# Kernel tuning notes

Hardware: AMD Instinct MI355X
Metric: run time of the kernel (lower is better)

Reference implementation:

```python
import math
import jax, jax.numpy as jnp
import numpy as np

B, T, C = 2, 2048, 1024
N_HEAD = 16
HEAD_DIM = C // N_HEAD


def setup_inputs() -> dict:
    key = jax.random.key(0)
    k1, k2, k3 = jax.random.split(key, 3)
    x = jax.random.normal(k1, (B, T, C), dtype=jnp.float32)
    w_attn = jax.random.normal(k2, (3 * C, C), dtype=jnp.float32) * 0.02
    w_proj = jax.random.normal(k3, (C, C), dtype=jnp.float32) * 0.02
    return {"x": x, "w_attn": w_attn, "w_proj": w_proj}


def _rope_cos_sin(seq_len, dim, dtype):
    inv_freq = 1.0 / (10000.0 ** (jnp.arange(0, dim, 2, dtype=jnp.float32) / dim))
    t = jnp.arange(seq_len, dtype=jnp.float32)
    freqs = jnp.einsum('i,j->ij', t, inv_freq)          # [T, dim/2]
    emb = jnp.concatenate([freqs, freqs], axis=-1)       # [T, dim]
    return jnp.cos(emb).astype(dtype), jnp.sin(emb).astype(dtype)


def _rotate_half(x):
    x1, x2 = jnp.split(x, 2, axis=-1)
    return jnp.concatenate([-x2, x1], axis=-1)


def _apply_rope(x, cos, sin):
    # x: [B, H, T, D]; cos/sin: [T, D] broadcast over batch/head
    return x * cos[None, None] + _rotate_half(x) * sin[None, None]


def reference(x, w_attn, w_proj):
    b, t, c = x.shape
    h, d = N_HEAD, c // N_HEAD
    qkv = x @ w_attn.T                                   # [B, T, 3C]
    q, k, v = jnp.split(qkv, 3, axis=-1)
    q = q.reshape(b, t, h, d).transpose(0, 2, 1, 3)      # [B, H, T, D]
    k = k.reshape(b, t, h, d).transpose(0, 2, 1, 3)
    v = v.reshape(b, t, h, d).transpose(0, 2, 1, 3)
    cos, sin = _rope_cos_sin(t, d, x.dtype)
    q = _apply_rope(q, cos, sin)
    k = _apply_rope(k, cos, sin)
    logits = jnp.einsum('bhqd,bhkd->bhqk', q, k) * (1.0 / math.sqrt(d))
    causal = jnp.tril(jnp.ones((t, t), dtype=bool))
    logits = jnp.where(causal[None, None], logits, jnp.float32(-jnp.inf).astype(logits.dtype))
    att = jax.nn.softmax(logits, axis=-1)                # [B, H, T, T]
    y = jnp.einsum('bhqk,bhkd->bhqd', att, v)            # [B, H, T, D]
    y = y.transpose(0, 2, 1, 3).reshape(b, t, c)
    return y @ w_proj.T
```

## Files before the change

kernel.cpp:

```cpp
#include <hip/hip_runtime.h>
#include <hip/hip_bf16.h>
#include <math.h>

#define B_ 2
#define T_ 2048
#define C_ 1024
#define H_ 16

typedef __bf16 bf16x8 __attribute__((ext_vector_type(8)));
typedef __bf16 bf16x4 __attribute__((ext_vector_type(4)));
typedef float f32x4 __attribute__((ext_vector_type(4)));
typedef float f32x16 __attribute__((ext_vector_type(16)));
typedef unsigned int u32;

#if __has_builtin(__builtin_amdgcn_exp2f)
#define EXP2(x) __builtin_amdgcn_exp2f(x)
#else
#define EXP2(x) exp2f(x)
#endif

__device__ __forceinline__ void gload16(const void* g, void* l) {
    __builtin_amdgcn_global_load_lds(
        (const __attribute__((address_space(1))) void*)g,
        (__attribute__((address_space(3))) void*)l, 16, 0, 0);
}

__device__ __forceinline__ f32x4 mfma16(bf16x8 a, bf16x8 b, f32x4 c) {
    return __builtin_amdgcn_mfma_f32_16x16x32_bf16(a, b, c, 0, 0, 0);
}
__device__ __forceinline__ f32x16 mfma32(bf16x8 a, bf16x8 b, f32x16 c) {
    return __builtin_amdgcn_mfma_f32_32x32x16_bf16(a, b, c, 0, 0, 0);
}

__device__ __forceinline__ u32 cvtpk(float lo, float hi) {
    u32 r;
    asm("v_cvt_pk_bf16_f32 %0, %1, %2" : "=v"(r) : "v"(lo), "v"(hi));
    return r;
}

__device__ __forceinline__ void plane32swap(u32& a, u32& b) {
#if __has_builtin(__builtin_amdgcn_permlane32_swap)
    auto r = __builtin_amdgcn_permlane32_swap(a, b, false, false);
    a = r[0]; b = r[1];
#else
    asm("v_permlane32_swap_b32 %0, %1" : "+v"(a), "+v"(b));
#endif
}

#define SCLQ 0.18033688011112042f
#define NLOG2_10K_32 (-0.4152410118609203f)

__global__ __launch_bounds__(256) void cast_all(const float* __restrict__ x,
                                                const float* __restrict__ wa,
                                                const float* __restrict__ wp,
                                                __bf16* __restrict__ xb,
                                                __bf16* __restrict__ wab,
                                                __bf16* __restrict__ wpb) {
    const int i = blockIdx.x * 256 + threadIdx.x;
    const float* src;
    __bf16* dst;
    int k;
    if (i < 1048576)               { src = x;  dst = xb;  k = i; }
    else if (i < 1048576 + 786432) { src = wa; dst = wab; k = i - 1048576; }
    else                           { src = wp; dst = wpb; k = i - (1048576 + 786432); }
    float4 v = ((const float4*)src)[k];
    bf16x4 o;
    o[0] = (__bf16)v.x; o[1] = (__bf16)v.y; o[2] = (__bf16)v.z; o[3] = (__bf16)v.w;
    ((bf16x4*)dst)[k] = o;
}

__global__ __launch_bounds__(256) void gemm_qkv(const __bf16* __restrict__ A,
                                                const __bf16* __restrict__ Bw,
                                                __bf16* __restrict__ Qb,
                                                __bf16* __restrict__ Kb,
                                                __bf16* __restrict__ Vt) {
    const int tid  = threadIdx.x;
    const int lane = tid & 63;
    const int w    = tid >> 6;
    const int wr = w >> 1, wc = w & 1;
    const int l15 = lane & 15, lg = lane >> 4;
    const int bm = blockIdx.y * 128, bn = blockIdx.x * 128;
    const int K = C_;
    __shared__ __bf16 Asm[128 * 64];
    __shared__ __bf16 Bsm[128 * 64];
    f32x4 acc[4][4] = {};

    for (int kt = 0; kt < K; kt += 64) {
        if (kt) __syncthreads();
#pragma unroll
        for (int it = 0; it < 4; ++it) {
            const int c = it * 256 + tid;
            const int row = c >> 3, cc = (c & 7) * 8;
            gload16(A  + (size_t)(bm + row) * K + kt + cc, Asm + c * 8);
            gload16(Bw + (size_t)(bn + row) * K + kt + cc, Bsm + c * 8);
        }
        __syncthreads();
#pragma unroll
        for (int kk = 0; kk < 64; kk += 32) {
            bf16x8 af[4], bf[4];
#pragma unroll
            for (int i = 0; i < 4; ++i)
                af[i] = *(const bf16x8*)&Asm[(wr * 64 + i * 16 + l15) * 64 + kk + lg * 8];
#pragma unroll
            for (int j = 0; j < 4; ++j)
                bf[j] = *(const bf16x8*)&Bsm[(wc * 64 + j * 16 + l15) * 64 + kk + lg * 8];
#pragma unroll
            for (int i = 0; i < 4; ++i)
#pragma unroll
                for (int j = 0; j < 4; ++j)
                    acc[i][j] = mfma16(af[i], bf[j], acc[i][j]);
        }
    }
    const int region  = bn >> 10;
    const int colbase = (bn & 1023) + wc * 64;
    const int h = colbase >> 6;
    if (region < 2) {
        __bf16* dst = region ? Kb : Qb;
        const float scl = region ? 1.0f : SCLQ;
#pragma unroll
        for (int j = 0; j < 2; ++j) {
            const int d = j * 16 + l15;
            const float invf = exp2f((float)d * NLOG2_10K_32);
#pragma unroll
            for (int i = 0; i < 4; ++i)
#pragma unroll
                for (int r = 0; r < 4; ++r) {
                    const int row = bm + wr * 64 + i * 16 + lg * 4 + r;
                    const int b = row >> 11, t = row & (T_ - 1);
                    float sv, cv;
                    __sincosf((float)t * invf, &sv, &cv);
                    const float v1 = acc[i][j][r], v2 = acc[i][j + 2][r];
                    const float o1 = (v1 * cv - v2 * sv) * scl;
                    const float o2 = (v2 * cv + v1 * sv) * scl;
                    const size_t base = ((size_t)(b * H_ + h) * T_ + t) * 64;
                    dst[base + d]      = (__bf16)o1;
                    dst[base + d + 32] = (__bf16)o2;
                }
        }
    } else {
#pragma unroll
        for (int i = 0; i < 4; ++i)
#pragma unroll
            for (int j = 0; j < 4; ++j) {
                const int vcol = colbase + j * 16 + l15;
                const int hh = vcol >> 6, d = vcol & 63;
                const int row0 = bm + wr * 64 + i * 16 + lg * 4;
                const int b = row0 >> 11, t0 = row0 & (T_ - 1);
                u32 dw[2];
                dw[0] = cvtpk(acc[i][j][0], acc[i][j][1]);
                dw[1] = cvtpk(acc[i][j][2], acc[i][j][3]);
                *(uint64_t*)&Vt[((size_t)(b * H_ + hh) * 64 + d) * T_ + t0] =
                    *(uint64_t*)dw;
            }
    }
}

__global__ __launch_bounds__(256) void gemm_proj(const __bf16* __restrict__ A,
                                                 const __bf16* __restrict__ Bw,
                                                 float* __restrict__ Cp,
                                                 int N, int K) {
    const int tid  = threadIdx.x;
    const int lane = tid & 63;
    const int w    = tid >> 6;
    const int wr = w >> 1, wc = w & 1;
    const int l15 = lane & 15, lg = lane >> 4;
    const int bm = blockIdx.y * 128, bn = blockIdx.x * 128;
    __shared__ __bf16 Asm[128 * 64];
    __shared__ __bf16 Bsm[128 * 64];
    f32x4 acc[4][4] = {};

    for (int kt = 0; kt < K; kt += 64) {
        if (kt) __syncthreads();
#pragma unroll
        for (int it = 0; it < 4; ++it) {
            const int c = it * 256 + tid;
            const int row = c >> 3, cc = (c & 7) * 8;
            gload16(A  + (size_t)(bm + row) * K + kt + cc, Asm + c * 8);
            gload16(Bw + (size_t)(bn + row) * K + kt + cc, Bsm + c * 8);
        }
        __syncthreads();
#pragma unroll
        for (int kk = 0; kk < 64; kk += 32) {
            bf16x8 af[4], bf[4];
#pragma unroll
            for (int i = 0; i < 4; ++i)
                af[i] = *(const bf16x8*)&Asm[(wr * 64 + i * 16 + l15) * 64 + kk + lg * 8];
#pragma unroll
            for (int j = 0; j < 4; ++j)
                bf[j] = *(const bf16x8*)&Bsm[(wc * 64 + j * 16 + l15) * 64 + kk + lg * 8];
#pragma unroll
            for (int i = 0; i < 4; ++i)
#pragma unroll
                for (int j = 0; j < 4; ++j)
                    acc[i][j] = mfma16(af[i], bf[j], acc[i][j]);
        }
    }
#pragma unroll
    for (int i = 0; i < 4; ++i)
#pragma unroll
        for (int j = 0; j < 4; ++j)
#pragma unroll
            for (int r = 0; r < 4; ++r) {
                const int row = bm + wr * 64 + i * 16 + lg * 4 + r;
                const int col = bn + wc * 64 + j * 16 + l15;
                Cp[(size_t)row * N + col] = acc[i][j][r];
            }
}

__global__ __launch_bounds__(256) void attn_fwd(const __bf16* __restrict__ Qb,
                                                const __bf16* __restrict__ Kb,
                                                const __bf16* __restrict__ Vt,
                                                __bf16* __restrict__ Yatt) {
    const int gid = blockIdx.x;
    const int bh = (gid & 7) * 4 + ((gid >> 3) & 3);
    const int qt = 15 - (gid >> 5);
    const int b = bh >> 4, h = bh & 15;
    const int tid = threadIdx.x, lane = tid & 63, w = tid >> 6;
    const int l31 = lane & 31, hi = lane >> 5;
    const int hi4 = hi * 4;
    __shared__ __bf16 Ksm[128 * 64];
    __shared__ __bf16 Vsm[64 * 128];

    const int Q0 = qt * 128 + w * 32;
    const int qg = Q0 + l31;
    const __bf16* Qp = Qb + ((size_t)bh * T_ + Q0) * 64;
    const __bf16* Kp = Kb + (size_t)bh * T_ * 64;
    const __bf16* Vp = Vt + (size_t)bh * 64 * T_;

    bf16x8 qf[4];
#pragma unroll
    for (int ds = 0; ds < 4; ++ds)
        qf[ds] = *(const bf16x8*)&Qp[l31 * 64 + ds * 16 + hi * 8];

    f32x16 ot[2] = {};
    float m_run = -1e30f, l_run = 0.f;

    const int jmax = qt + 1;
    for (int j = 0; j < jmax; ++j) {
        __syncthreads();
#pragma unroll
        for (int it = 0; it < 4; ++it) {
            const int g = it * 256 + tid;
            const int kr = g >> 3, kc = (g & 7) ^ (kr & 7);
            gload16(Kp + ((size_t)(j * 128 + kr)) * 64 + kc * 8, Ksm + g * 8);
            const int vd = g >> 4, vg = (g & 15) ^ (vd & 15);
            gload16(Vp + (size_t)vd * T_ + j * 128 + vg * 8, Vsm + g * 8);
        }
        __syncthreads();

        f32x16 st[4] = {};
#pragma unroll
        for (int a = 0; a < 4; ++a)
#pragma unroll
            for (int ds = 0; ds < 4; ++ds) {
                const int row = a * 32 + l31;
                const int off = (ds * 32 + hi * 16) ^ ((row & 7) << 4);
                bf16x8 kf = *(const bf16x8*)((const char*)Ksm + row * 128 + off);
                st[a] = mfma32(kf, qf[ds], st[a]);
            }
        if (j == qt) {
#pragma unroll
            for (int a = 0; a < 4; ++a)
#pragma unroll
                for (int r = 0; r < 16; ++r) {
                    const int kv = j * 128 + a * 32 + (r & 3) + 8 * (r >> 2) + hi4;
                    if (kv > qg) st[a][r] = -1e30f;
                }
        }
        float t8[8];
#pragma unroll
        for (int i = 0; i < 8; ++i)
            t8[i] = fmaxf(fmaxf(fmaxf(st[0][i], st[0][i + 8]),
                                fmaxf(st[1][i], st[1][i + 8])),
                          fmaxf(fmaxf(st[2][i], st[2][i + 8]),
                                fmaxf(st[3][i], st[3][i + 8])));
        float mx = fmaxf(fmaxf(fmaxf(t8[0], t8[1]), fmaxf(t8[2], t8[3])),
                         fmaxf(fmaxf(t8[4], t8[5]), fmaxf(t8[6], t8[7])));
        mx = fmaxf(mx, __shfl_xor(mx, 32));
        if (!__all(mx - m_run <= 10.f)) {
            const float mnew = fmaxf(m_run, mx);
            const float corr = EXP2(m_run - mnew);
            l_run *= corr;
#pragma unroll
            for (int db = 0; db < 2; ++db)
#pragma unroll
                for (int r = 0; r < 16; ++r) ot[db][r] *= corr;
            m_run = mnew;
        }
        float s0 = 0.f, s1 = 0.f;
#pragma unroll
        for (int a = 0; a < 4; ++a)
#pragma unroll
            for (int r = 0; r < 16; ++r) {
                const float e = EXP2(st[a][r] - m_run);
                st[a][r] = e;
                if (r & 1) s1 += e; else s0 += e;
            }
        float rs = s0 + s1;
        rs += __shfl_xor(rs, 32);
        l_run += rs;
        bf16x8 pa[8];
#pragma unroll
        for (int ks = 0; ks < 8; ++ks) {
            const int a = ks >> 1, rb = (ks & 1) * 8;
            u32 X0 = cvtpk(st[a][rb + 0], st[a][rb + 1]);
            u32 X1 = cvtpk(st[a][rb + 2], st[a][rb + 3]);
            u32 Y0 = cvtpk(st[a][rb + 4], st[a][rb + 5]);
            u32 Y1 = cvtpk(st[a][rb + 6], st[a][rb + 7]);
            plane32swap(X0, Y0);
            plane32swap(X1, Y1);
            u32 dw[4] = {X0, X1, Y0, Y1};
            pa[ks] = *(bf16x8*)dw;
        }
#pragma unroll
        for (int ks = 0; ks < 8; ++ks)
#pragma unroll
            for (int db = 0; db < 2; ++db) {
                const int row = db * 32 + l31;
                const int off = ((ks * 2 + hi) ^ (row & 15)) * 16;
                bf16x8 vf = *(const bf16x8*)((const char*)Vsm + row * 256 + off);
                ot[db] = mfma32(vf, pa[ks], ot[db]);
            }
    }
    const float inv = 1.f / l_run;
    __bf16* Yp = Yatt + ((size_t)(b * T_ + qg)) * C_ + h * 64;
#pragma unroll
    for (int db = 0; db < 2; ++db)
#pragma unroll
        for (int rq = 0; rq < 4; ++rq) {
            const int r = rq * 4;
            u32 dw[2];
            dw[0] = cvtpk(ot[db][r] * inv,     ot[db][r + 1] * inv);
            dw[1] = cvtpk(ot[db][r + 2] * inv, ot[db][r + 3] * inv);
            const int d = db * 32 + 8 * rq + hi4;
            *(uint64_t*)&Yp[d] = *(uint64_t*)dw;
        }
}

extern "C" void kernel_launch(void* const* d_in, const int* in_sizes, int n_in,
                              void* d_out, int out_size, void* d_ws, size_t ws_size,
                              hipStream_t stream) {
    const float* x      = (const float*)d_in[0];
    const float* w_attn = (const float*)d_in[1];
    const float* w_proj = (const float*)d_in[2];
    float* out = (float*)d_out;
    char* ws = (char*)d_ws;

    __bf16* xb  = (__bf16*)(ws);
    __bf16* wab = (__bf16*)(ws + 8388608);
    __bf16* wpb = (__bf16*)(ws + 14680064);
    __bf16* Qb  = (__bf16*)(ws + 16777216);
    __bf16* Kb  = (__bf16*)(ws + 25165824);
    __bf16* Vt  = (__bf16*)(ws + 33554432);
    __bf16* Ya  = (__bf16*)(ws + 41943040);

    cast_all<<<dim3(8192), 256, 0, stream>>>(x, w_attn, w_proj, xb, wab, wpb);

    gemm_qkv<<<dim3(3 * C_ / 128, B_ * T_ / 128), 256, 0, stream>>>(
        xb, wab, Qb, Kb, Vt);

    attn_fwd<<<dim3(16 * 32), 256, 0, stream>>>(Qb, Kb, Vt, Ya);

    gemm_proj<<<dim3(C_ / 128, B_ * T_ / 128), 256, 0, stream>>>(
        Ya, wpb, out, C_, C_);
}
```

Baseline: 111.4 us.

## Double-buffer K/V tiles in attention, rebalance q-tile order, shrink proj GEMM tile

The attention kernel now keeps two LDS buffers for K and V and prefetches the next key block while the current one is computed, using explicit vmcnt waits and raw barriers in place of full syncthreads. Query-tile scheduling changes from strictly longest-first to a mix of long and short tiles, to even out the causal workload across waves of blocks. The output projection GEMM uses 64-row M tiles, doubling the grid to 512 blocks so more CUs are busy. The costs are twice the LDS per attention block, which can lower occupancy, and less reuse of each B tile in the projection GEMM.

New measurement: 108.9 us. 2.2% less time.

```diff
diff --git a/kernel.cpp b/kernel.cpp
--- a/kernel.cpp
+++ b/kernel.cpp
@@ -164,44 +164,49 @@
     const int w    = tid >> 6;
     const int wr = w >> 1, wc = w & 1;
     const int l15 = lane & 15, lg = lane >> 4;
-    const int bm = blockIdx.y * 128, bn = blockIdx.x * 128;
-    __shared__ __bf16 Asm[128 * 64];
+    const int bm = blockIdx.y * 64, bn = blockIdx.x * 128;
+    __shared__ __bf16 Asm[64 * 64];
     __shared__ __bf16 Bsm[128 * 64];
-    f32x4 acc[4][4] = {};
+    f32x4 acc[2][4] = {};
 
     for (int kt = 0; kt < K; kt += 64) {
         if (kt) __syncthreads();
 #pragma unroll
+        for (int it = 0; it < 2; ++it) {
+            const int g = it * 256 + tid;
+            const int row = g >> 3, cc = (g & 7) * 8;
+            gload16(A + (size_t)(bm + row) * K + kt + cc, Asm + g * 8);
+        }
+#pragma unroll
         for (int it = 0; it < 4; ++it) {
-            const int c = it * 256 + tid;
-            const int row = c >> 3, cc = (c & 7) * 8;
-            gload16(A  + (size_t)(bm + row) * K + kt + cc, Asm + c * 8);
-            gload16(Bw + (size_t)(bn + row) * K + kt + cc, Bsm + c * 8);
+            const int g = it * 256 + tid;
+            const int row = g >> 3, cc = (g & 7) * 8;
+            gload16(Bw + (size_t)(bn + row) * K + kt + cc, Bsm + g * 8);
         }
         __syncthreads();
 #pragma unroll
         for (int kk = 0; kk < 64; kk += 32) {
-            bf16x8 af[4], bf[4];
-#pragma unroll
-            for (int i = 0; i < 4; ++i)
-                af[i] = *(const bf16x8*)&Asm[(wr * 64 + i * 16 + l15) * 64 + kk + lg * 8];
+            bf16x8 af[2], bf[4];
+#pragma unroll
+            for (int i = 0; i < 2; ++i)
+                af[i] = *(const bf16x8*)&Asm[(wr * 32 + i * 16 + l15) * 64 + kk + lg * 8];
 #pragma unroll
             for (int j = 0; j < 4; ++j)
                 bf[j] = *(const bf16x8*)&Bsm[(wc * 64 + j * 16 + l15) * 64 + kk + lg * 8];
 #pragma unroll
-            for (int i = 0; i < 4; ++i)
+            for (int i = 0; i < 2; ++i)
 #pragma unroll
                 for (int j = 0; j < 4; ++j)
                     acc[i][j] = mfma16(af[i], bf[j], acc[i][j]);
         }
     }
 #pragma unroll
-    for (int i = 0; i < 4; ++i)
+    for (int i = 0; i < 2; ++i)
 #pragma unroll
         for (int j = 0; j < 4; ++j)
 #pragma unroll
             for (int r = 0; r < 4; ++r) {
-                const int row = bm + wr * 64 + i * 16 + lg * 4 + r;
+                const int row = bm + wr * 32 + i * 16 + lg * 4 + r;
                 const int col = bn + wc * 64 + j * 16 + l15;
                 Cp[(size_t)row * N + col] = acc[i][j][r];
             }
@@ -213,13 +218,14 @@
                                                 __bf16* __restrict__ Yatt) {
     const int gid = blockIdx.x;
     const int bh = (gid & 7) * 4 + ((gid >> 3) & 3);
-    const int qt = 15 - (gid >> 5);
+    const int qq = gid >> 5;
+    const int qt = (qq < 8) ? (15 - qq) : (qq - 8);
     const int b = bh >> 4, h = bh & 15;
     const int tid = threadIdx.x, lane = tid & 63, w = tid >> 6;
     const int l31 = lane & 31, hi = lane >> 5;
     const int hi4 = hi * 4;
-    __shared__ __bf16 Ksm[128 * 64];
-    __shared__ __bf16 Vsm[64 * 128];
+    __shared__ __bf16 Ksm[2][128 * 64];
+    __shared__ __bf16 Vsm[2][64 * 128];
 
     const int Q0 = qt * 128 + w * 32;
     const int qg = Q0 + l31;
@@ -227,26 +233,41 @@
     const __bf16* Kp = Kb + (size_t)bh * T_ * 64;
     const __bf16* Vp = Vt + (size_t)bh * 64 * T_;
 
-    bf16x8 qf[4];
-#pragma unroll
-    for (int ds = 0; ds < 4; ++ds)
-        qf[ds] = *(const bf16x8*)&Qp[l31 * 64 + ds * 16 + hi * 8];
-
-    f32x16 ot[2] = {};
-    float m_run = -1e30f, l_run = 0.f;
-
-    const int jmax = qt + 1;
-    for (int j = 0; j < jmax; ++j) {
-        __syncthreads();
+    auto STAGE = [&](int j) {
+        __bf16* Ks = Ksm[j & 1];
+        __bf16* Vs = Vsm[j & 1];
 #pragma unroll
         for (int it = 0; it < 4; ++it) {
             const int g = it * 256 + tid;
             const int kr = g >> 3, kc = (g & 7) ^ (kr & 7);
-            gload16(Kp + ((size_t)(j * 128 + kr)) * 64 + kc * 8, Ksm + g * 8);
+            gload16(Kp + ((size_t)(j * 128 + kr)) * 64 + kc * 8, Ks + g * 8);
             const int vd = g >> 4, vg = (g & 15) ^ (vd & 15);
-            gload16(Vp + (size_t)vd * T_ + j * 128 + vg * 8, Vsm + g * 8);
-        }
-        __syncthreads();
+            gload16(Vp + (size_t)vd * T_ + j * 128 + vg * 8, Vs + g * 8);
+        }
+    };
+
+    const int jmax = qt + 1;
+    STAGE(0);
+
+    bf16x8 qf[4];
+#pragma unroll
+    for (int ds = 0; ds < 4; ++ds)
+        qf[ds] = *(const bf16x8*)&Qp[l31 * 64 + ds * 16 + hi * 8];
+
+    f32x16 ot[2] = {};
+    float m_run = -1e30f, l_run = 0.f;
+
+    for (int j = 0; j < jmax; ++j) {
+        const int cur = j & 1;
+        __builtin_amdgcn_s_barrier();
+        if (j + 1 < jmax) {
+            STAGE(j + 1);
+            asm volatile("s_waitcnt vmcnt(8)" ::: "memory");
+        } else {
+            asm volatile("s_waitcnt vmcnt(0)" ::: "memory");
+        }
+        __builtin_amdgcn_s_barrier();
+        __builtin_amdgcn_sched_barrier(0);
 
         f32x16 st[4] = {};
 #pragma unroll
@@ -255,7 +276,7 @@
             for (int ds = 0; ds < 4; ++ds) {
                 const int row = a * 32 + l31;
                 const int off = (ds * 32 + hi * 16) ^ ((row & 7) << 4);
-                bf16x8 kf = *(const bf16x8*)((const char*)Ksm + row * 128 + off);
+                bf16x8 kf = *(const bf16x8*)((const char*)Ksm[cur] + row * 128 + off);
                 st[a] = mfma32(kf, qf[ds], st[a]);
             }
         if (j == qt) {
@@ -318,7 +339,7 @@
             for (int db = 0; db < 2; ++db) {
                 const int row = db * 32 + l31;
                 const int off = ((ks * 2 + hi) ^ (row & 15)) * 16;
-                bf16x8 vf = *(const bf16x8*)((const char*)Vsm + row * 256 + off);
+                bf16x8 vf = *(const bf16x8*)((const char*)Vsm[cur] + row * 256 + off);
                 ot[db] = mfma32(vf, pa[ks], ot[db]);
             }
     }
@@ -361,6 +382,6 @@
 
     attn_fwd<<<dim3(16 * 32), 256, 0, stream>>>(Qb, Kb, Vt, Ya);
 
-    gemm_proj<<<dim3(C_ / 128, B_ * T_ / 128), 256, 0, stream>>>(
+    gemm_proj<<<dim3(C_ / 128, B_ * T_ / 64), 256, 0, stream>>>(
         Ya, wpb, out, C_, C_);
 }
```
